# Optimization experiments

Measured on AMD Instinct MI355X. Metric: run time of the kernel, lower is better.

The kernel has to match this reference:

```python
import jax, jax.numpy as jnp
import numpy as np

D_MODEL = 1024
N_HEADS = 16
HEAD_DIM = D_MODEL // N_HEADS
NEG = -10000.0  # module uses -10000, not -inf


def setup_inputs() -> dict:
    key = jax.random.key(0)
    ks = jax.random.split(key, 8)
    B, T = 4, 2048
    q = jax.random.normal(ks[0], (B, T, D_MODEL), dtype=jnp.float32)
    k = jax.random.normal(ks[1], (B, T, D_MODEL), dtype=jnp.float32)
    v = jax.random.normal(ks[2], (B, T, D_MODEL), dtype=jnp.float32)
    attn_mask = jnp.ones((B, T), dtype=jnp.float32)
    # xavier_uniform for square [d, d] weights: limit = sqrt(6/(d+d))
    lim = float(np.sqrt(6.0 / (D_MODEL + D_MODEL)))
    Wq = jax.random.uniform(ks[3], (D_MODEL, D_MODEL), jnp.float32, -lim, lim)
    Wk = jax.random.uniform(ks[4], (D_MODEL, D_MODEL), jnp.float32, -lim, lim)
    Wv = jax.random.uniform(ks[5], (D_MODEL, D_MODEL), jnp.float32, -lim, lim)
    Wo = jax.random.uniform(ks[6], (D_MODEL, D_MODEL), jnp.float32, -lim, lim)
    return {"q": q, "k": k, "v": v, "attn_mask": attn_mask,
            "Wq": Wq, "Wk": Wk, "Wv": Wv, "Wo": Wo, "mask_future": 1}


def _split_heads(x):
    B, T, _ = x.shape
    return x.reshape(B, T, N_HEADS, HEAD_DIM).transpose(0, 2, 1, 3)  # [B,H,T,D]


def reference(q, k, v, attn_mask, Wq, Wk, Wv, Wo, mask_future):
    # torch Linear: y = x @ W.T  (weights stored [out, in])
    qh = _split_heads(jnp.einsum('btd,ed->bte', q, Wq))
    kh = _split_heads(jnp.einsum('btd,ed->bte', k, Wk))
    vh = _split_heads(jnp.einsum('btd,ed->bte', v, Wv))
    L, S = qh.shape[-2], kh.shape[-2]
    # dual scale: each of q and k scaled by 1/d**0.25
    scale = 1.0 / jnp.sqrt(jnp.sqrt(jnp.float32(HEAD_DIM)))
    scores = jnp.einsum('bhld,bhsd->bhls', qh * scale, kh * scale)
    if mask_future:
        causal_bias = jnp.triu(jnp.full((L, S), NEG, dtype=scores.dtype), k=1)
        scores = scores + causal_bias
    # padding mask: attn_mask [B, S] -> broadcast [B,1,1,S]; 0 entries -> -10000
    pad = attn_mask[:, None, None, :]
    scores = jnp.where(pad == 0, jnp.asarray(NEG, scores.dtype), scores)
    probs = jax.nn.softmax(scores, axis=-1)  # dropout p=0.0 -> identity
    ctx = jnp.einsum('bhls,bhsd->bhld', probs, vh)
    B = ctx.shape[0]
    ctx = ctx.transpose(0, 2, 1, 3).reshape(B, L, D_MODEL)
    return jnp.einsum('btd,ed->bte', ctx, Wo)
```

## Files before the change

kernel.cpp:

```cpp
#include <hip/hip_runtime.h>

typedef unsigned short u16;
typedef __attribute__((ext_vector_type(8))) _Float16 f16x8;
typedef __attribute__((ext_vector_type(2))) __fp16 fp16v2;
typedef __attribute__((ext_vector_type(4))) float f32x4;
typedef __attribute__((ext_vector_type(16))) float f32x16;

#define T_SEQ 2048
#define NH 16
#define DH 64
#define DM 1024
#define NEG2 (-14426.95f)
#define QS2 (0.42466089f)

__device__ __forceinline__ unsigned pk2(float a, float b) {
  union { fp16v2 v; unsigned u; } c;
  c.v = __builtin_amdgcn_cvt_pkrtz(a, b);
  return c.u;
}
__device__ __forceinline__ u16 f2h(float a) {
  union { _Float16 h; u16 u; } c; c.h = (_Float16)a; return c.u;
}

__device__ __forceinline__ void async_load16(const void* g, void* l) {
  __builtin_amdgcn_global_load_lds(
      (const __attribute__((address_space(1))) unsigned int*)(g),
      (__attribute__((address_space(3))) unsigned int*)(l), 16, 0, 0);
}

__global__ __launch_bounds__(256) void convert_all(
    const float* __restrict__ q, const float* __restrict__ k, const float* __restrict__ v,
    const float* __restrict__ Wq, const float* __restrict__ Wk, const float* __restrict__ Wv,
    const float* __restrict__ Wo, u16* __restrict__ xb, u16* __restrict__ wb) {
  int blk = blockIdx.x;
  const float* src; u16* dst;
  if (blk < 12288) {
    int s = blk >> 12;
    src = (s == 0) ? q : (s == 1) ? k : v;
    dst = xb + (size_t)s * 8388608u;
    blk &= 4095;
  } else {
    int s = (blk - 12288) >> 9;
    src = (s == 0) ? Wq : (s == 1) ? Wk : (s == 2) ? Wv : Wo;
    dst = wb + (size_t)s * 1048576u;
    blk = (blk - 12288) & 511;
  }
  size_t base = (size_t)blk * 2048 + (size_t)threadIdx.x * 8;
  float4 a = *(const float4*)(src + base);
  float4 b2 = *(const float4*)(src + base + 4);
  uint4 st;
  st.x = pk2(a.x, a.y); st.y = pk2(a.z, a.w);
  st.z = pk2(b2.x, b2.y); st.w = pk2(b2.z, b2.w);
  *(uint4*)(dst + base) = st;
}

__global__ __launch_bounds__(512) void gemm_qkv(const u16* __restrict__ A,
                                                const u16* __restrict__ Wqb,
                                                const u16* __restrict__ Wkb,
                                                const u16* __restrict__ Wvb,
                                                u16* __restrict__ Qh, u16* __restrict__ Kh,
                                                u16* __restrict__ VTh) {
  __shared__ char lds[147456];
  const int tid = threadIdx.x;
  const int wid = tid >> 6, lane = tid & 63;
  const int l32 = lane & 31, lh = lane >> 5;
  const int m0 = blockIdx.x * 256;
  const int n0 = blockIdx.y * 128;
  const int which = n0 >> 10;
  const int n0l = n0 & 1023;
  const u16* As = A + (size_t)which * 8388608u;
  const u16* Bw = (which == 0) ? Wqb : (which == 1) ? Wkb : Wvb;
  f32x16 acc[2][2] = {};

  const u16* gsrc[6]; int ldso[6];
#pragma unroll
  for (int u = 0; u < 6; ++u) {
    int c = wid * 6 + u;
    ldso[u] = c * 1024;
    if (c < 32)
      gsrc[u] = As + (size_t)(m0 + (c >> 2) * 32 + l32) * 1024 + (c & 3) * 16 + lh * 8;
    else {
      int cw = c - 32;
      gsrc[u] = Bw + (size_t)(n0l + (cw >> 2) * 32 + l32) * 1024 + (cw & 3) * 16 + lh * 8;
    }
  }

  const int rOff = (which < 2) ? 32768 : 0;
  const int cOff = 32768 - rOff;
  const int rgo = (which < 2) ? ((wid & 1) * 2) : ((wid >> 1) * 2);
  const int cgo = (which < 2) ? ((wid >> 1) * 2) : ((wid & 1) * 2);

#pragma unroll
  for (int u = 0; u < 6; ++u) async_load16(gsrc[u] + 0 * 64, lds + 0 * 49152 + ldso[u]);
#pragma unroll
  for (int u = 0; u < 6; ++u) async_load16(gsrc[u] + 1 * 64, lds + 1 * 49152 + ldso[u]);
  asm volatile("s_waitcnt vmcnt(6)" ::: "memory");
  __builtin_amdgcn_s_barrier();
  asm volatile("" ::: "memory");

  int slotc = 0, slotn = 2;
  for (int kt = 0; kt < 16; ++kt) {
    char* bufc = lds + slotc * 49152;
    char* bufn = lds + slotn * 49152;
    const char* rb = bufc + rOff;
    const char* cb = bufc + cOff;
    f16x8 a0[4], a1[4], b0[4], b1[4];
#pragma unroll
    for (int k = 0; k < 4; ++k) {
      a0[k] = *(const f16x8*)(rb + ((rgo + 0) * 4 + k) * 1024 + lane * 16);
      b0[k] = *(const f16x8*)(cb + ((cgo + 0) * 4 + k) * 1024 + lane * 16);
      b1[k] = *(const f16x8*)(cb + ((cgo + 1) * 4 + k) * 1024 + lane * 16);
    }
    if (kt < 14) {
#pragma unroll
      for (int u = 0; u < 3; ++u) async_load16(gsrc[u] + (kt + 2) * 64, bufn + ldso[u]);
    }
    asm volatile("" ::: "memory");
    __builtin_amdgcn_s_barrier();
    asm volatile("s_waitcnt lgkmcnt(0)" ::: "memory");
    __builtin_amdgcn_sched_barrier(0);
    __builtin_amdgcn_s_setprio(1);
#pragma unroll
    for (int k = 0; k < 4; ++k) {
      acc[0][0] = __builtin_amdgcn_mfma_f32_32x32x16_f16(a0[k], b0[k], acc[0][0], 0, 0, 0);
      acc[0][1] = __builtin_amdgcn_mfma_f32_32x32x16_f16(a0[k], b1[k], acc[0][1], 0, 0, 0);
    }
    __builtin_amdgcn_s_setprio(0);
    asm volatile("" ::: "memory");
    __builtin_amdgcn_s_barrier();
#pragma unroll
    for (int k = 0; k < 4; ++k)
      a1[k] = *(const f16x8*)(rb + ((rgo + 1) * 4 + k) * 1024 + lane * 16);
    if (kt < 14) {
#pragma unroll
      for (int u = 3; u < 6; ++u) async_load16(gsrc[u] + (kt + 2) * 64, bufn + ldso[u]);
    }
    if (kt < 14) asm volatile("s_waitcnt vmcnt(6)" ::: "memory");
    else         asm volatile("s_waitcnt vmcnt(0)" ::: "memory");
    asm volatile("" ::: "memory");
    __builtin_amdgcn_s_barrier();
    asm volatile("s_waitcnt lgkmcnt(0)" ::: "memory");
    __builtin_amdgcn_sched_barrier(0);
    __builtin_amdgcn_s_setprio(1);
#pragma unroll
    for (int k = 0; k < 4; ++k) {
      acc[1][0] = __builtin_amdgcn_mfma_f32_32x32x16_f16(a1[k], b0[k], acc[1][0], 0, 0, 0);
      acc[1][1] = __builtin_amdgcn_mfma_f32_32x32x16_f16(a1[k], b1[k], acc[1][1], 0, 0, 0);
    }
    __builtin_amdgcn_s_setprio(0);
    asm volatile("" ::: "memory");
    __builtin_amdgcn_s_barrier();
    slotc = (slotc == 2) ? 0 : slotc + 1;
    slotn = (slotn == 2) ? 0 : slotn + 1;
  }

  const float s = (which < 2) ? QS2 : 1.0f;
  const int b = m0 >> 11, t0 = m0 & 2047, h0 = n0l >> 6;
  __syncthreads();
  if (which < 2) {
#pragma unroll
    for (int i = 0; i < 2; ++i)
#pragma unroll
      for (int j = 0; j < 2; ++j) {
        int colb = (wid >> 1) * 64 + j * 32 + l32;
        int rowb = (wid & 1) * 64 + i * 32 + 4 * lh;
#pragma unroll
        for (int g = 0; g < 4; ++g) {
          uint2 pv;
          pv.x = pk2(acc[i][j][4 * g + 0] * s, acc[i][j][4 * g + 1] * s);
          pv.y = pk2(acc[i][j][4 * g + 2] * s, acc[i][j][4 * g + 3] * s);
          *(uint2*)(lds + colb * 264 + (rowb + 8 * g) * 2) = pv;
        }
      }
    __syncthreads();
    u16* O = which ? Kh : Qh;
#pragma unroll
    for (int p = 0; p < 8; ++p) {
      int row = p * 32 + (tid >> 4);
      int seg = tid & 15;
      uint4 val = *(const uint4*)(lds + row * 264 + seg * 16);
      int hl = seg >> 3, dh0 = (seg & 7) * 8;
      *(uint4*)(O + (((size_t)(b * NH + h0 + hl) * T_SEQ + t0 + row) << 6) + dh0) = val;
    }
  } else {
#pragma unroll
    for (int i = 0; i < 2; ++i)
#pragma unroll
      for (int j = 0; j < 2; ++j) {
        int colb = (wid & 1) * 64 + j * 32 + l32;
        int rowb = (wid >> 1) * 64 + i * 32 + 4 * lh;
#pragma unroll
        for (int g = 0; g < 4; ++g) {
          uint2 pv;
          pv.x = pk2(acc[i][j][4 * g + 0], acc[i][j][4 * g + 1]);
          pv.y = pk2(acc[i][j][4 * g + 2], acc[i][j][4 * g + 3]);
          *(uint2*)(lds + colb * 520 + (rowb + 8 * g) * 2) = pv;
        }
      }
    __syncthreads();
#pragma unroll
    for (int p = 0; p < 8; ++p) {
      int row = p * 16 + (tid >> 5);
      int seg = tid & 31;
      uint4 val = *(const uint4*)(lds + row * 520 + seg * 16);
      int h = h0 + (row >> 6), dh = row & 63;
      *(uint4*)(VTh + (((size_t)(b * NH + h) * DH + dh) << 11) + t0 + seg * 8) = val;
    }
  }
}

__global__ __launch_bounds__(256) void gemm_out(const u16* __restrict__ A,
                                                const u16* __restrict__ Bw,
                                                float* __restrict__ O) {
  __shared__ char lds[49152];
  const int tid = threadIdx.x;
  const int wid = tid >> 6, lane = tid & 63;
  const int l32 = lane & 31, lh = lane >> 5;
  const int m0 = blockIdx.x * 128, n0 = blockIdx.y * 128;
  const int wm = wid >> 1, wn = wid & 1;
  f32x16 acc[2][2] = {};

  const u16* gA = A + (size_t)(m0 + wid * 32 + l32) * 1024 + lh * 8;
  const u16* gB = Bw + (size_t)(n0 + wid * 32 + l32) * 1024 + lh * 8;
  for (int t = 0; t < 2; ++t) {
    char* bf = lds + t * 16384;
    async_load16(gA + t * 32, bf + (wid * 2 + 0) * 1024);
    async_load16(gA + t * 32 + 16, bf + (wid * 2 + 1) * 1024);
    async_load16(gB + t * 32, bf + 8192 + (wid * 2 + 0) * 1024);
    async_load16(gB + t * 32 + 16, bf + 8192 + (wid * 2 + 1) * 1024);
  }

  int buf = 0;
  for (int it = 0; it < 32; ++it) {
    if (it < 31) asm volatile("s_waitcnt vmcnt(4)" ::: "memory");
    else         asm volatile("s_waitcnt vmcnt(0)" ::: "memory");
    __builtin_amdgcn_s_barrier();
    asm volatile("" ::: "memory");
    char* cur = lds + buf * 16384;
    if (it < 30) {
      char* nxt = lds + ((buf == 0) ? 2 : buf - 1) * 16384;
      int kt = (it + 2) * 32;
      async_load16(gA + kt, nxt + (wid * 2 + 0) * 1024);
      async_load16(gA + kt + 16, nxt + (wid * 2 + 1) * 1024);
      async_load16(gB + kt, nxt + 8192 + (wid * 2 + 0) * 1024);
      async_load16(gB + kt + 16, nxt + 8192 + (wid * 2 + 1) * 1024);
    }
    f16x8 af0[2], bf0[2], af1[2], bf1[2];
    for (int i = 0; i < 2; ++i) {
      af0[i] = *(const f16x8*)(cur + ((wm * 2 + i) * 2 + 0) * 1024 + lane * 16);
      bf0[i] = *(const f16x8*)(cur + 8192 + ((wn * 2 + i) * 2 + 0) * 1024 + lane * 16);
    }
    for (int i = 0; i < 2; ++i) {
      af1[i] = *(const f16x8*)(cur + ((wm * 2 + i) * 2 + 1) * 1024 + lane * 16);
      bf1[i] = *(const f16x8*)(cur + 8192 + ((wn * 2 + i) * 2 + 1) * 1024 + lane * 16);
    }
    for (int i = 0; i < 2; ++i)
      for (int j = 0; j < 2; ++j)
        acc[i][j] = __builtin_amdgcn_mfma_f32_32x32x16_f16(af0[i], bf0[j], acc[i][j], 0, 0, 0);
    for (int i = 0; i < 2; ++i)
      for (int j = 0; j < 2; ++j)
        acc[i][j] = __builtin_amdgcn_mfma_f32_32x32x16_f16(af1[i], bf1[j], acc[i][j], 0, 0, 0);
    buf = (buf == 2) ? 0 : buf + 1;
  }
  for (int i = 0; i < 2; ++i)
    for (int j = 0; j < 2; ++j) {
      int col = n0 + wn * 64 + j * 32 + l32;
      int rowb = m0 + wm * 64 + i * 32 + 4 * lh;
      for (int g = 0; g < 4; ++g)
        for (int rr = 0; rr < 4; ++rr)
          O[(size_t)(rowb + 8 * g + rr) * 1024 + col] = acc[i][j][4 * g + rr];
    }
}

__global__ __launch_bounds__(512) void attn_kernel(const u16* __restrict__ Qh,
                                                   const u16* __restrict__ Kh,
                                                   const u16* __restrict__ VTh,
                                                   const float* __restrict__ attn_mask,
                                                   const int* __restrict__ mfp,
                                                   u16* __restrict__ ctx) {
  __shared__ char kls[2][8192];
  __shared__ char vls[2][8192];
  __shared__ char pls[8][2048];
  __shared__ float maskb[T_SEQ];
  __shared__ int mzf;

  const int tid = threadIdx.x;
  const int wid = tid >> 6, lane = tid & 63;
  const int lm = lane & 15, lq = lane >> 4;
  const int bid = blockIdx.x;
  const int bh_i = bid & 63, p8 = bid >> 6;
  const int b = bh_i >> 4, h = bh_i & 15;
  const int mf = *mfp;
  const size_t bh = (size_t)(b * NH + h);
  const u16* Qbh = Qh + bh * T_SEQ * DH;
  const u16* Kbh = Kh + bh * T_SEQ * DH;
  const u16* VTbh = VTh + bh * DH * T_SEQ;

  if (tid == 0) mzf = 0;
  __syncthreads();
  {
    int az = 0;
    for (int i = tid; i < T_SEQ; i += 512) {
      float mv = attn_mask[(size_t)b * T_SEQ + i];
      maskb[i] = (mv == 0.0f) ? NEG2 : 0.0f;
      az |= (mv == 0.0f);
    }
    if (az) mzf = 1;
  }
  __syncthreads();
  const int maskzero = mzf;

  for (int half = 0; half < 2; ++half) {
    const int qt = half ? (15 - p8) : p8;
    const int q0 = qt * 128;
    const int qw = q0 + wid * 16;
    f16x8 qf[2];
    qf[0] = *(const f16x8*)(Qbh + (size_t)(qw + lm) * DH + lq * 8);
    qf[1] = *(const f16x8*)(Qbh + (size_t)(qw + lm) * DH + 32 + lq * 8);

    f32x4 acc[4] = {};
    float mprev = -1e30f, lsum = 0.f;

    const int nch = mf ? (qt + 1) * 2 : 32;
    __syncthreads();
    {
      async_load16(Kbh + (size_t)((wid >> 1) * 16 + lm) * DH + (wid & 1) * 32 + lq * 8,
                   kls[0] + wid * 1024);
      async_load16(VTbh + (size_t)((wid >> 1) * 16 + lm) * T_SEQ + (wid & 1) * 32 + lq * 8,
                   vls[0] + wid * 1024);
    }
    for (int c = 0; c < nch; ++c) {
      const int s0 = c * 64;
      asm volatile("s_waitcnt vmcnt(0)" ::: "memory");
      __builtin_amdgcn_s_barrier();
      asm volatile("" ::: "memory");
      if (c + 1 < nch) {
        const int s1 = s0 + 64;
        async_load16(Kbh + (size_t)(s1 + (wid >> 1) * 16 + lm) * DH + (wid & 1) * 32 + lq * 8,
                     kls[(c + 1) & 1] + wid * 1024);
        async_load16(VTbh + (size_t)((wid >> 1) * 16 + lm) * T_SEQ + s1 + (wid & 1) * 32 + lq * 8,
                     vls[(c + 1) & 1] + wid * 1024);
      }
      const char* kcur = kls[c & 1];
      const char* vcur = vls[c & 1];

      f32x4 sc[4];
      for (int st = 0; st < 4; ++st) {
        f32x4 z = {0.f, 0.f, 0.f, 0.f};
        sc[st] = z;
        for (int kk = 0; kk < 2; ++kk) {
          f16x8 kf = *(const f16x8*)(kcur + ((st * 2 + kk) * 64 + lane) * 16);
          sc[st] = __builtin_amdgcn_mfma_f32_16x16x32_f16(kf, qf[kk], sc[st], 0, 0, 0);
        }
      }
      if (maskzero) {
        for (int st = 0; st < 4; ++st) {
          f32x4 mb = *(const f32x4*)(maskb + s0 + st * 16 + lq * 4);
          for (int r = 0; r < 4; ++r) sc[st][r] += mb[r];
        }
      }
      if (mf && (s0 + 64 > qw)) {
        int qg = qw + lm;
        for (int st = 0; st < 4; ++st)
          for (int r = 0; r < 4; ++r)
            if (s0 + st * 16 + lq * 4 + r > qg) sc[st][r] = NEG2;
      }
      float mx = fmaxf(fmaxf(sc[0][0], sc[0][1]), fmaxf(sc[0][2], sc[0][3]));
      for (int st = 1; st < 4; ++st) {
        float t2 = fmaxf(fmaxf(sc[st][0], sc[st][1]), fmaxf(sc[st][2], sc[st][3]));
        mx = fmaxf(mx, t2);
      }
      mx = fmaxf(mx, __shfl_xor(mx, 16));
      mx = fmaxf(mx, __shfl_xor(mx, 32));
      float mn = mprev;
      if (__ballot(mx > mprev) != 0ull) {
        mn = fmaxf(mprev, mx);
        float alpha = exp2f(mprev - mn);
        for (int r = 0; r < 4; ++r) {
          float ar = __shfl(alpha, lq * 4 + r);
          for (int nt = 0; nt < 4; ++nt) acc[nt][r] *= ar;
        }
        lsum *= alpha;
        mprev = mn;
      }
      float ps = 0.f;
      for (int st = 0; st < 4; ++st)
        for (int r = 0; r < 4; ++r) {
          float p = exp2f(sc[st][r] - mn);
          sc[st][r] = p;
          ps += p;
        }
      ps += __shfl_xor(ps, 16);
      ps += __shfl_xor(ps, 32);
      lsum += ps;
      {
        char* pw = pls[wid];
        for (int st = 0; st < 4; ++st) {
          int kk = st >> 1;
          int lqp = (st & 1) * 2 + (lq >> 1);
          uint2 pv;
          pv.x = pk2(sc[st][0], sc[st][1]);
          pv.y = pk2(sc[st][2], sc[st][3]);
          *(uint2*)(pw + kk * 1024 + (lqp * 16 + lm) * 16 + (lq & 1) * 8) = pv;
        }
      }
      asm volatile("s_waitcnt lgkmcnt(0)" ::: "memory");
      for (int kk = 0; kk < 2; ++kk) {
        f16x8 pf = *(const f16x8*)(pls[wid] + kk * 1024 + lane * 16);
        for (int nt = 0; nt < 4; ++nt) {
          f16x8 vf = *(const f16x8*)(vcur + ((nt * 2 + kk) * 64 + lane) * 16);
          acc[nt] = __builtin_amdgcn_mfma_f32_16x16x32_f16(pf, vf, acc[nt], 0, 0, 0);
        }
      }
    }
    float inv = 1.0f / lsum;
    for (int r = 0; r < 4; ++r) {
      float ir = __shfl(inv, lq * 4 + r);
      int t = qw + lq * 4 + r;
      for (int nt = 0; nt < 4; ++nt)
        ctx[((size_t)(b * T_SEQ + t) * DM) + h * DH + nt * 16 + lm] = f2h(acc[nt][r] * ir);
    }
  }
}

extern "C" void kernel_launch(void* const* d_in, const int* in_sizes, int n_in,
                              void* d_out, int out_size, void* d_ws, size_t ws_size,
                              hipStream_t stream) {
  const float* q = (const float*)d_in[0];
  const float* k = (const float*)d_in[1];
  const float* v = (const float*)d_in[2];
  const float* attn_mask = (const float*)d_in[3];
  const float* Wq = (const float*)d_in[4];
  const float* Wk = (const float*)d_in[5];
  const float* Wv = (const float*)d_in[6];
  const float* Wo = (const float*)d_in[7];
  const int* mf = (const int*)d_in[8];

  u16* ws = (u16*)d_ws;
  u16* qb  = ws;
  u16* wqb = ws + 3u * 8388608u;
  u16* wkb = wqb + 1048576u;
  u16* wvb = wkb + 1048576u;
  u16* wob = wvb + 1048576u;
  u16* Qh  = wob + 1048576u;
  u16* Kh  = Qh + 8388608u;
  u16* VTh = Kh + 8388608u;
  u16* ctxb = ws;

  convert_all<<<14336, 256, 0, stream>>>(q, k, v, Wq, Wk, Wv, Wo, qb, wqb);

  dim3 gq(32, 24);
  gemm_qkv<<<gq, 512, 0, stream>>>(qb, wqb, wkb, wvb, Qh, Kh, VTh);

  attn_kernel<<<512, 512, 0, stream>>>(Qh, Kh, VTh, attn_mask, mf, ctxb);

  dim3 gg(64, 8);
  gemm_out<<<gg, 256, 0, stream>>>(ctxb, wob, (float*)d_out);
}
```

Measured before the change: 359.5 us.

## Restructure output GEMM into 256x128 tiles with ping-pong MFMA scheduling; lazy softmax rescale

Rewrites gemm_out to use 512-thread blocks over 256x128 tiles with K-step 64 and triple-buffered 48KB LDS stages. The loads and the two MFMA halves are interleaved with barriers, sched_barrier and setprio, so global loads overlap tensor-core work and fewer blocks are launched. In attention, the running max is reduced with a shallower tree, and the rescale is skipped unless the new max beats the old one by more than 8 (in log2 units). That lazy rescale lowers the cost of the alpha correction but lets exponentials grow up to 2^8 before normalisation, which adds some fp16 precision risk in P. The large LDS allocation (144KB) limits occupancy to one block per CU.

```diff
diff --git a/kernel.cpp b/kernel.cpp
--- a/kernel.cpp
+++ b/kernel.cpp
@@ -209,64 +209,102 @@
   }
 }
 
-__global__ __launch_bounds__(256) void gemm_out(const u16* __restrict__ A,
+__global__ __launch_bounds__(512) void gemm_out(const u16* __restrict__ A,
                                                 const u16* __restrict__ Bw,
                                                 float* __restrict__ O) {
-  __shared__ char lds[49152];
+  __shared__ char lds[147456];
   const int tid = threadIdx.x;
   const int wid = tid >> 6, lane = tid & 63;
   const int l32 = lane & 31, lh = lane >> 5;
-  const int m0 = blockIdx.x * 128, n0 = blockIdx.y * 128;
-  const int wm = wid >> 1, wn = wid & 1;
+  const int m0 = blockIdx.x * 256, n0 = blockIdx.y * 128;
   f32x16 acc[2][2] = {};
 
-  const u16* gA = A + (size_t)(m0 + wid * 32 + l32) * 1024 + lh * 8;
-  const u16* gB = Bw + (size_t)(n0 + wid * 32 + l32) * 1024 + lh * 8;
-  for (int t = 0; t < 2; ++t) {
-    char* bf = lds + t * 16384;
-    async_load16(gA + t * 32, bf + (wid * 2 + 0) * 1024);
-    async_load16(gA + t * 32 + 16, bf + (wid * 2 + 1) * 1024);
-    async_load16(gB + t * 32, bf + 8192 + (wid * 2 + 0) * 1024);
-    async_load16(gB + t * 32 + 16, bf + 8192 + (wid * 2 + 1) * 1024);
-  }
-
-  int buf = 0;
-  for (int it = 0; it < 32; ++it) {
-    if (it < 31) asm volatile("s_waitcnt vmcnt(4)" ::: "memory");
+  const u16* gsrc[6]; int ldso[6];
+#pragma unroll
+  for (int u = 0; u < 6; ++u) {
+    int c = wid * 6 + u;
+    ldso[u] = c * 1024;
+    if (c < 32)
+      gsrc[u] = A + (size_t)(m0 + (c >> 2) * 32 + l32) * 1024 + (c & 3) * 16 + lh * 8;
+    else {
+      int cw = c - 32;
+      gsrc[u] = Bw + (size_t)(n0 + (cw >> 2) * 32 + l32) * 1024 + (cw & 3) * 16 + lh * 8;
+    }
+  }
+  const int rgo = (wid >> 1) * 2, cgo = (wid & 1) * 2;
+
+#pragma unroll
+  for (int u = 0; u < 6; ++u) async_load16(gsrc[u] + 0 * 64, lds + 0 * 49152 + ldso[u]);
+#pragma unroll
+  for (int u = 0; u < 6; ++u) async_load16(gsrc[u] + 1 * 64, lds + 1 * 49152 + ldso[u]);
+  asm volatile("s_waitcnt vmcnt(6)" ::: "memory");
+  __builtin_amdgcn_s_barrier();
+  asm volatile("" ::: "memory");
+
+  int slotc = 0, slotn = 2;
+  for (int kt = 0; kt < 16; ++kt) {
+    char* bufc = lds + slotc * 49152;
+    char* bufn = lds + slotn * 49152;
+    const char* rb = bufc;
+    const char* cb = bufc + 32768;
+    f16x8 a0[4], a1[4], b0[4], b1[4];
+#pragma unroll
+    for (int k = 0; k < 4; ++k) {
+      a0[k] = *(const f16x8*)(rb + ((rgo + 0) * 4 + k) * 1024 + lane * 16);
+      b0[k] = *(const f16x8*)(cb + ((cgo + 0) * 4 + k) * 1024 + lane * 16);
+      b1[k] = *(const f16x8*)(cb + ((cgo + 1) * 4 + k) * 1024 + lane * 16);
+    }
+    if (kt < 14) {
+#pragma unroll
+      for (int u = 0; u < 3; ++u) async_load16(gsrc[u] + (kt + 2) * 64, bufn + ldso[u]);
+    }
+    asm volatile("" ::: "memory");
+    __builtin_amdgcn_s_barrier();
+    asm volatile("s_waitcnt lgkmcnt(0)" ::: "memory");
+    __builtin_amdgcn_sched_barrier(0);
+    __builtin_amdgcn_s_setprio(1);
+#pragma unroll
+    for (int k = 0; k < 4; ++k) {
+      acc[0][0] = __builtin_amdgcn_mfma_f32_32x32x16_f16(a0[k], b0[k], acc[0][0], 0, 0, 0);
+      acc[0][1] = __builtin_amdgcn_mfma_f32_32x32x16_f16(a0[k], b1[k], acc[0][1], 0, 0, 0);
+    }
+    __builtin_amdgcn_s_setprio(0);
+    asm volatile("" ::: "memory");
+    __builtin_amdgcn_s_barrier();
+#pragma unroll
+    for (int k = 0; k < 4; ++k)
+      a1[k] = *(const f16x8*)(rb + ((rgo + 1) * 4 + k) * 1024 + lane * 16);
+    if (kt < 14) {
+#pragma unroll
+      for (int u = 3; u < 6; ++u) async_load16(gsrc[u] + (kt + 2) * 64, bufn + ldso[u]);
+    }
+    if (kt < 14) asm volatile("s_waitcnt vmcnt(6)" ::: "memory");
     else         asm volatile("s_waitcnt vmcnt(0)" ::: "memory");
-    __builtin_amdgcn_s_barrier();
-    asm volatile("" ::: "memory");
-    char* cur = lds + buf * 16384;
-    if (it < 30) {
-      char* nxt = lds + ((buf == 0) ? 2 : buf - 1) * 16384;
-      int kt = (it + 2) * 32;
-      async_load16(gA + kt, nxt + (wid * 2 + 0) * 1024);
-      async_load16(gA + kt + 16, nxt + (wid * 2 + 1) * 1024);
-      async_load16(gB + kt, nxt + 8192 + (wid * 2 + 0) * 1024);
-      async_load16(gB + kt + 16, nxt + 8192 + (wid * 2 + 1) * 1024);
-    }
-    f16x8 af0[2], bf0[2], af1[2], bf1[2];
-    for (int i = 0; i < 2; ++i) {
-      af0[i] = *(const f16x8*)(cur + ((wm * 2 + i) * 2 + 0) * 1024 + lane * 16);
-      bf0[i] = *(const f16x8*)(cur + 8192 + ((wn * 2 + i) * 2 + 0) * 1024 + lane * 16);
-    }
-    for (int i = 0; i < 2; ++i) {
-      af1[i] = *(const f16x8*)(cur + ((wm * 2 + i) * 2 + 1) * 1024 + lane * 16);
-      bf1[i] = *(const f16x8*)(cur + 8192 + ((wn * 2 + i) * 2 + 1) * 1024 + lane * 16);
-    }
-    for (int i = 0; i < 2; ++i)
-      for (int j = 0; j < 2; ++j)
-        acc[i][j] = __builtin_amdgcn_mfma_f32_32x32x16_f16(af0[i], bf0[j], acc[i][j], 0, 0, 0);
-    for (int i = 0; i < 2; ++i)
-      for (int j = 0; j < 2; ++j)
-        acc[i][j] = __builtin_amdgcn_mfma_f32_32x32x16_f16(af1[i], bf1[j], acc[i][j], 0, 0, 0);
-    buf = (buf == 2) ? 0 : buf + 1;
-  }
+    asm volatile("" ::: "memory");
+    __builtin_amdgcn_s_barrier();
+    asm volatile("s_waitcnt lgkmcnt(0)" ::: "memory");
+    __builtin_amdgcn_sched_barrier(0);
+    __builtin_amdgcn_s_setprio(1);
+#pragma unroll
+    for (int k = 0; k < 4; ++k) {
+      acc[1][0] = __builtin_amdgcn_mfma_f32_32x32x16_f16(a1[k], b0[k], acc[1][0], 0, 0, 0);
+      acc[1][1] = __builtin_amdgcn_mfma_f32_32x32x16_f16(a1[k], b1[k], acc[1][1], 0, 0, 0);
+    }
+    __builtin_amdgcn_s_setprio(0);
+    asm volatile("" ::: "memory");
+    __builtin_amdgcn_s_barrier();
+    slotc = (slotc == 2) ? 0 : slotc + 1;
+    slotn = (slotn == 2) ? 0 : slotn + 1;
+  }
+#pragma unroll
   for (int i = 0; i < 2; ++i)
+#pragma unroll
     for (int j = 0; j < 2; ++j) {
-      int col = n0 + wn * 64 + j * 32 + l32;
-      int rowb = m0 + wm * 64 + i * 32 + 4 * lh;
+      int col = n0 + (wid & 1) * 64 + j * 32 + l32;
+      int rowb = m0 + (wid >> 1) * 64 + i * 32 + 4 * lh;
+#pragma unroll
       for (int g = 0; g < 4; ++g)
+#pragma unroll
         for (int rr = 0; rr < 4; ++rr)
           O[(size_t)(rowb + 8 * g + rr) * 1024 + col] = acc[i][j][4 * g + rr];
     }
@@ -365,28 +403,28 @@
           for (int r = 0; r < 4; ++r)
             if (s0 + st * 16 + lq * 4 + r > qg) sc[st][r] = NEG2;
       }
-      float mx = fmaxf(fmaxf(sc[0][0], sc[0][1]), fmaxf(sc[0][2], sc[0][3]));
-      for (int st = 1; st < 4; ++st) {
-        float t2 = fmaxf(fmaxf(sc[st][0], sc[st][1]), fmaxf(sc[st][2], sc[st][3]));
-        mx = fmaxf(mx, t2);
-      }
+      float u0 = fmaxf(fmaxf(sc[0][0], sc[0][1]), sc[0][2]);
+      float u1 = fmaxf(fmaxf(sc[0][3], sc[1][0]), sc[1][1]);
+      float u2 = fmaxf(fmaxf(sc[1][2], sc[1][3]), sc[2][0]);
+      float u3 = fmaxf(fmaxf(sc[2][1], sc[2][2]), sc[2][3]);
+      float u4 = fmaxf(fmaxf(sc[3][0], sc[3][1]), sc[3][2]);
+      float mx = fmaxf(fmaxf(fmaxf(u0, u1), u2), fmaxf(fmaxf(u3, u4), sc[3][3]));
       mx = fmaxf(mx, __shfl_xor(mx, 16));
       mx = fmaxf(mx, __shfl_xor(mx, 32));
-      float mn = mprev;
-      if (__ballot(mx > mprev) != 0ull) {
-        mn = fmaxf(mprev, mx);
-        float alpha = exp2f(mprev - mn);
+      if (__ballot(mx > mprev + 8.0f) != 0ull) {
+        float mn2 = fmaxf(mprev, mx);
+        float alpha = exp2f(mprev - mn2);
         for (int r = 0; r < 4; ++r) {
           float ar = __shfl(alpha, lq * 4 + r);
           for (int nt = 0; nt < 4; ++nt) acc[nt][r] *= ar;
         }
         lsum *= alpha;
-        mprev = mn;
+        mprev = mn2;
       }
       float ps = 0.f;
       for (int st = 0; st < 4; ++st)
         for (int r = 0; r < 4; ++r) {
-          float p = exp2f(sc[st][r] - mn);
+          float p = exp2f(sc[st][r] - mprev);
           sc[st][r] = p;
           ps += p;
         }
@@ -454,6 +492,6 @@
 
   attn_kernel<<<512, 512, 0, stream>>>(Qh, Kh, VTh, attn_mask, mf, ctxb);
 
-  dim3 gg(64, 8);
-  gemm_out<<<gg, 256, 0, stream>>>(ctxb, wob, (float*)d_out);
-}
+  dim3 gg(32, 8);
+  gemm_out<<<gg, 512, 0, stream>>>(ctxb, wob, (float*)d_out);
+}
```

New measurement: 348.5 us. -3.1%, faster.
